# Kernel tuning notes

Measured on AMD Instinct MI355X. Metric: run time of the kernel, lower is better.

The kernel has to match this reference:

```python
import jax, jax.numpy as jnp
import numpy as np

B, M, K = 32768, 8192, 16
EPS = 1e-5  # torch BatchNorm1d default


def _bn_relu(x, g, b):
    # training-mode batch norm (biased variance), matching torch BatchNorm1d forward
    m = x.mean(0)
    v = x.var(0)
    return jax.nn.relu(g * (x - m) * jax.lax.rsqrt(v + EPS) + b)


def _forward(pos, mc, mv, w1, b1, w2, b2, w3, b3, w4, b4, w5, b5, w6, b6,
             g1, be1, g2, be2, g3, be3, g4, be4, g5, be5, k):
    # squared pairwise distances [B, M]; same ordering as L2 norm used by torch.sort
    d2 = (pos * pos).sum(1, keepdims=True) + (mc * mc).sum(1)[None, :] - 2.0 * (pos @ mc.T)
    _, idx = jax.lax.top_k(-d2, k)                     # k nearest indices [B, k]
    nb = jnp.concatenate([mc[idx], mv[idx]], axis=-1)  # [B, k, 4] = (coord, value) per neighbor
    knn_feat = jnp.concatenate([pos, nb.reshape(pos.shape[0], k * 4)], axis=1)  # [B, 2+4k]
    x = _bn_relu(knn_feat @ w1 + b1, g1, be1)
    x = _bn_relu(x @ w2 + b2, g2, be2)
    x = _bn_relu(x @ w3 + b3, g3, be3)
    x = _bn_relu(x @ w4 + b4, g4, be4)
    x = _bn_relu(x @ w5 + b5, g5, be5)  # dropout = identity (eval mode)
    x = x @ w6 + b6
    return x, knn_feat


def setup_inputs() -> dict:
    key = jax.random.key(0)
    ks = jax.random.split(key, 32)
    d_in = 2 + K * 4
    dims = [(d_in, 128), (128, 256), (256, 512), (512, 128), (128, 64), (64, 2)]
    inp = {
        "pos": jax.random.normal(ks[0], (B, 2), jnp.float32),
        "measure_coords": jax.random.normal(ks[1], (M, 2), jnp.float32),
        "measure_vals": jax.random.normal(ks[2], (M, 2), jnp.float32),
    }
    for i, (fi, fo) in enumerate(dims, 1):
        inp[f"w{i}"] = jax.random.normal(ks[2 + 2 * i], (fi, fo), jnp.float32) / np.float32(np.sqrt(fi))
        inp[f"b{i}"] = jnp.zeros((fo,), jnp.float32)
    for i, n in enumerate([128, 256, 512, 128, 64], 1):
        inp[f"g{i}"] = jnp.ones((n,), jnp.float32)
        inp[f"be{i}"] = jnp.zeros((n,), jnp.float32)
    inp["k"] = K
    return inp


def reference(pos, measure_coords, measure_vals, w1, b1, w2, b2, w3, b3, w4, b4,
              w5, b5, w6, b6, g1, be1, g2, be2, g3, be3, g4, be4, g5, be5, k):
    return _forward(pos, measure_coords, measure_vals, w1, b1, w2, b2, w3, b3, w4,
                    b4, w5, b5, w6, b6, g1, be1, g2, be2, g3, be3, g4, be4, g5, be5, k)
```

## Files before the change

### kernel.cpp

```cpp
#include <hip/hip_runtime.h>

typedef unsigned short u16;
typedef unsigned int   u32;
typedef __attribute__((ext_vector_type(8))) short bf16x8;
typedef __attribute__((ext_vector_type(4))) float f32x4;

#define B_ROWS 32768
#define EPS_BN 1e-5f

__device__ __forceinline__ u16 f2bf(float f) {
  u32 u = __float_as_uint(f);
  u32 r = (u + 0x7FFFu + ((u >> 16) & 1u)) >> 16;
  return (u16)r;
}
__device__ __forceinline__ u32 pk2bf(float a, float b) {
  return (u32)f2bf(a) | ((u32)f2bf(b) << 16);
}
__device__ __forceinline__ float bf2f(u16 h) {
  return __uint_as_float(((u32)h) << 16);
}

__device__ __forceinline__ float dcalc(float px, float py, float sp, float mx, float my) {
#pragma clang fp contract(off)
  float sm   = mx * mx + my * my;
  float pm   = px * mx;
  float dot  = __builtin_fmaf(py, my, pm);
  float spsm = sp + sm;
  return __builtin_fmaf(dot, -2.0f, spsm);
}
__device__ __forceinline__ float dcalc2(float px, float py, float sp, float mx, float my,
                                        float sm) {
#pragma clang fp contract(off)
  float pm   = px * mx;
  float dot  = __builtin_fmaf(py, my, pm);
  float spsm = sp + sm;
  return __builtin_fmaf(dot, -2.0f, spsm);
}
__device__ __forceinline__ float smcalc(float mx, float my) {
#pragma clang fp contract(off)
  return mx * mx + my * my;
}
__device__ __forceinline__ float spcalc(float px, float py) {
#pragma clang fp contract(off)
  return px * px + py * py;
}
#define MED3 __builtin_amdgcn_fmed3f

__global__ __launch_bounds__(256, 8)
void knn_kernel(const float2* __restrict__ pos, const float2* __restrict__ mc,
                const float2* __restrict__ mv, float* __restrict__ knn_out,
                u16* __restrict__ X0)
{
  __shared__ float tv[16 * 130];
  __shared__ float tstS[16];
  __shared__ float qxS[16], qyS[16], qsS[16];
  __shared__ unsigned long long qmaskS[16];
  __shared__ int   qcnt[16];
  __shared__ int   ntaskS;

  const int t = threadIdx.x;
  const int g = t >> 6;
  const int s = t & 63;
  const int q0 = blockIdx.x * 16;

  float px[4], py[4], sp[4];
#pragma unroll
  for (int j = 0; j < 4; ++j) {
    float2 p = pos[q0 + g * 4 + j];
    px[j] = p.x; py[j] = p.y; sp[j] = spcalc(p.x, p.y);
  }
#pragma unroll
  for (int j = 0; j < 4; ++j) {
    if (s == j) { qxS[g * 4 + j] = px[j]; qyS[g * 4 + j] = py[j]; qsS[g * 4 + j] = sp[j]; }
  }

  const float4* mc4 = (const float4*)mc;

  float z0[4], z1[4];
#pragma unroll
  for (int j = 0; j < 4; ++j) { z0[j] = __builtin_inff(); z1[j] = __builtin_inff(); }

  float4 cur = mc4[s];
  for (int i = 0; i < 64; ++i) {
    float4 nxt = mc4[((i + 1) & 63) * 64 + s];
    float smA = smcalc(cur.x, cur.y);
    float smB = smcalc(cur.z, cur.w);
#pragma unroll
    for (int j = 0; j < 4; ++j) {
      float dA = dcalc2(px[j], py[j], sp[j], cur.x, cur.y, smA);
      z1[j] = MED3(z0[j], dA, z1[j]); z0[j] = fminf(z0[j], dA);
      float dB = dcalc2(px[j], py[j], sp[j], cur.z, cur.w, smB);
      z1[j] = MED3(z0[j], dB, z1[j]); z0[j] = fminf(z0[j], dB);
    }
    cur = nxt;
  }
#pragma unroll
  for (int j = 0; j < 4; ++j) {
    float2 zz; zz.x = z0[j]; zz.y = z1[j];
    *(float2*)(&tv[(g * 4 + j) * 130 + s * 2]) = zz;
  }
  __syncthreads();

  if (t < 16) {
    float ch[16];
#pragma unroll
    for (int j = 0; j < 16; ++j) ch[j] = __builtin_inff();
    for (int k = 0; k < 128; ++k) {
      float v = tv[t * 130 + k];
#pragma unroll
      for (int j = 15; j >= 1; --j) ch[j] = MED3(ch[j-1], v, ch[j]);
      ch[0] = fminf(ch[0], v);
    }
    tstS[t] = ch[15];
    qcnt[t] = 0;
    if (t == 0) ntaskS = 0;
  }
  __syncthreads();

  {
    float Tq[4];
#pragma unroll
    for (int j = 0; j < 4; ++j) Tq[j] = tstS[g * 4 + j];
    unsigned long long m;
#pragma unroll
    for (int j = 0; j < 4; ++j) {
      m = __ballot(z0[j] <= Tq[j]);
      if (s == j) qmaskS[g * 4 + j] = m;
    }
  }
  __syncthreads();

  u16* qcand = (u16*)tv;
  u16* taskS = ((u16*)tv) + 1024;
  if (t < 16) {
    unsigned long long m = qmaskS[t];
    int c = __popcll(m);
    int off = atomicAdd(&ntaskS, c);
    u16 qb = (u16)(t << 6);
    while (m) {
      int b = (int)__builtin_ctzll(m);
      m &= m - 1;
      taskS[off++] = qb | (u16)b;
    }
  }
  __syncthreads();

  const int ntask = ntaskS;
  for (int i0 = t; i0 < ntask; i0 += 256) {
    const int task = taskS[i0];
    const int qrow = task >> 6;
    const int sl   = task & 63;
    const float qx = qxS[qrow], qy = qyS[qrow];
    const float qs = qsS[qrow], qT = tstS[qrow];
#pragma unroll 4
    for (int i = 0; i < 64; ++i) {
      float4 c2 = mc4[i * 64 + sl];
      const int pidx = 2 * (i * 64 + sl);
      float smA = smcalc(c2.x, c2.y);
      float smB = smcalc(c2.z, c2.w);
      float dA = dcalc2(qx, qy, qs, c2.x, c2.y, smA);
      float dB = dcalc2(qx, qy, qs, c2.z, c2.w, smB);
      if (dA <= qT) {
        int o = atomicAdd(&qcnt[qrow], 1);
        if (o < 64) qcand[qrow * 64 + o] = (u16)pidx;
      }
      if (dB <= qT) {
        int o = atomicAdd(&qcnt[qrow], 1);
        if (o < 64) qcand[qrow * 64 + o] = (u16)(pidx + 1);
      }
    }
  }
  __syncthreads();

  if (t < 16) {
    const int q = q0 + t;
    float2 p = pos[q];
    const float sq = spcalc(p.x, p.y);
    int cnt = qcnt[t]; if (cnt > 64) cnt = 64;
    float fd[16]; int fi[16];
#pragma unroll
    for (int j = 0; j < 16; ++j) { fd[j] = __builtin_inff(); fi[j] = 0x7fffffff; }
    for (int j = 0; j < cnt; ++j) {
      int ci = qcand[t * 64 + j];
      float2 m = mc[ci];
      float d = dcalc(p.x, p.y, sq, m.x, m.y);
      bool cc = (d < fd[15]) || (d == fd[15] && ci < fi[15]);
      if (cc) {
#pragma unroll
        for (int k = 15; k >= 1; --k) {
          bool cm = (d < fd[k-1]) || (d == fd[k-1] && ci < fi[k-1]);
          if (cc) {
            if (cm) { fd[k] = fd[k-1]; fi[k] = fi[k-1]; }
            else    { fd[k] = d;       fi[k] = ci;      }
          }
          cc = cm;
        }
        if (cc) { fd[0] = d; fi[0] = ci; }
      }
    }
    float* orow = knn_out + (size_t)q * 66;
    u16*   xrow = X0 + (size_t)q * 96;
    float2 pp; pp.x = p.x; pp.y = p.y;
    *(float2*)(&orow[0]) = pp;
    *(u32*)(&xrow[0]) = pk2bf(p.x, p.y);
#pragma unroll
    for (int j = 0; j < 16; ++j) {
      int ci = fi[j];
      float2 m = mc[ci], v = mv[ci];
      *(float2*)(&orow[2 + 4*j]) = m;
      *(float2*)(&orow[4 + 4*j]) = v;
      *(u32*)(&xrow[2 + 4*j]) = pk2bf(m.x, m.y);
      *(u32*)(&xrow[4 + 4*j]) = pk2bf(v.x, v.y);
    }
#pragma unroll
    for (int c = 33; c < 48; ++c) ((u32*)xrow)[c] = 0;
  }
}

__global__ __launch_bounds__(256)
void prep_wt_all(const float* __restrict__ w1, const float* __restrict__ w2,
                 const float* __restrict__ w3, const float* __restrict__ w4,
                 const float* __restrict__ w5,
                 u16* __restrict__ wt1, u16* __restrict__ wt2, u16* __restrict__ wt3,
                 u16* __restrict__ wt4, u16* __restrict__ wt5)
{
  const int l = blockIdx.y;
  const float* w; u16* wt; int K, N, Kp;
  if (l == 0)      { w = w1; wt = wt1; K = 66;  N = 128; Kp = 96;  }
  else if (l == 1) { w = w2; wt = wt2; K = 128; N = 256; Kp = 128; }
  else if (l == 2) { w = w3; wt = wt3; K = 256; N = 512; Kp = 256; }
  else if (l == 3) { w = w4; wt = wt4; K = 512; N = 128; Kp = 512; }
  else             { w = w5; wt = wt5; K = 128; N = 64;  Kp = 128; }
  int i = blockIdx.x * 256 + threadIdx.x;
  if (i >= N * Kp) return;
  int n = i / Kp, kp = i - n * Kp;
  float v = (kp < K) ? w[(size_t)kp * N + n] : 0.0f;
  wt[i] = f2bf(v);
}

template<int BN, bool FUSE>
__global__ __launch_bounds__(256)
void gemm_bn_kernel(const u16* __restrict__ X, int Kw,
                    const u16* __restrict__ WT,
                    const float* __restrict__ bias,
                    const float* __restrict__ psum, const float* __restrict__ psq,
                    const float* __restrict__ gw,   const float* __restrict__ bw,
                    u16* __restrict__ Z, int N,
                    float* __restrict__ csum, float* __restrict__ csq)
{
  constexpr int BM = 128;
  constexpr int AST = 40;
  __shared__ u16 Ash[BM * AST];
  __shared__ u16 Bsh[BN * AST];
  __shared__ float redS[4][BN];
  __shared__ float redQ[4][BN];
  __shared__ float scA[512];
  __shared__ float ttA[512];

  const int t = threadIdx.x;
  const int wave = t >> 6;
  const int lane = t & 63;
  const int lr = lane & 15;
  const int qd = lane >> 4;
  const int m0 = blockIdx.x * BM;
  const int n0 = blockIdx.y * BN;

  if (FUSE) {
    const float invB = 1.0f / 32768.0f;
    for (int c = t; c < Kw; c += 256) {
      float mean = psum[c] * invB;
      float var  = __fmaf_rn(-mean, mean, psq[c] * invB);
      float sc   = gw[c] * rsqrtf(var + EPS_BN);
      scA[c] = sc;
      ttA[c] = __fmaf_rn(-mean, sc, bw[c]);
    }
    __syncthreads();
  }

  f32x4 acc[2][BN / 16];
#pragma unroll
  for (int a = 0; a < 2; ++a)
#pragma unroll
    for (int b = 0; b < BN / 16; ++b) {
      acc[a][b][0] = 0.f; acc[a][b][1] = 0.f; acc[a][b][2] = 0.f; acc[a][b][3] = 0.f;
    }

  const int sr = t >> 2;
  const int sk = (t & 3) * 8;

  for (int k0 = 0; k0 < Kw; k0 += 32) {
#pragma unroll
    for (int rr = 0; rr < 2; ++rr) {
      int r = sr + rr * 64;
      uint4 g = *(const uint4*)(&X[(size_t)(m0 + r) * Kw + k0 + sk]);
      if (FUSE) {
        u32 w[4] = {g.x, g.y, g.z, g.w};
        u32 o[4];
#pragma unroll
        for (int e = 0; e < 4; ++e) {
          int kk = k0 + sk + 2 * e;
          float lo = bf2f((u16)(w[e] & 0xffffu));
          float hi = bf2f((u16)(w[e] >> 16));
          float yl = fmaxf(__fmaf_rn(lo, scA[kk],     ttA[kk]),     0.0f);
          float yh = fmaxf(__fmaf_rn(hi, scA[kk + 1], ttA[kk + 1]), 0.0f);
          o[e] = (u32)f2bf(yl) | ((u32)f2bf(yh) << 16);
        }
        g.x = o[0]; g.y = o[1]; g.z = o[2]; g.w = o[3];
      }
      *(uint4*)(&Ash[r * AST + sk]) = g;
    }
    if (BN == 128) {
#pragma unroll
      for (int rr = 0; rr < 2; ++rr) {
        int n = sr + rr * 64;
        *(uint4*)(&Bsh[n * AST + sk]) =
            *(const uint4*)(&WT[(size_t)(n0 + n) * Kw + k0 + sk]);
      }
    } else {
      int n = sr;
      *(uint4*)(&Bsh[n * AST + sk]) =
          *(const uint4*)(&WT[(size_t)(n0 + n) * Kw + k0 + sk]);
    }
    __syncthreads();
    bf16x8 af0 = *(const bf16x8*)(&Ash[(wave * 32 + lr) * AST + qd * 8]);
    bf16x8 af1 = *(const bf16x8*)(&Ash[(wave * 32 + 16 + lr) * AST + qd * 8]);
#pragma unroll
    for (int ct = 0; ct < BN / 16; ++ct) {
      bf16x8 bfr = *(const bf16x8*)(&Bsh[(ct * 16 + lr) * AST + qd * 8]);
      acc[0][ct] = __builtin_amdgcn_mfma_f32_16x16x32_bf16(af0, bfr, acc[0][ct], 0, 0, 0);
      acc[1][ct] = __builtin_amdgcn_mfma_f32_16x16x32_bf16(af1, bfr, acc[1][ct], 0, 0, 0);
    }
    __syncthreads();
  }

#pragma unroll
  for (int ct = 0; ct < BN / 16; ++ct) {
    int cg = n0 + ct * 16 + lr;
    float bv = bias[cg];
    float s = 0.f, sqv = 0.f;
#pragma unroll
    for (int rt = 0; rt < 2; ++rt) {
#pragma unroll
      for (int r = 0; r < 4; ++r) {
        float z = acc[rt][ct][r] + bv;
        int row = m0 + wave * 32 + rt * 16 + qd * 4 + r;
        Z[(size_t)row * N + cg] = f2bf(z);
        s += z;
        sqv = __fmaf_rn(z, z, sqv);
      }
    }
    s   += __shfl_xor(s, 16);   s   += __shfl_xor(s, 32);
    sqv += __shfl_xor(sqv, 16); sqv += __shfl_xor(sqv, 32);
    if (qd == 0) { redS[wave][ct * 16 + lr] = s; redQ[wave][ct * 16 + lr] = sqv; }
  }
  __syncthreads();
  if (t < BN) {
    float s  = redS[0][t] + redS[1][t] + redS[2][t] + redS[3][t];
    float sv = redQ[0][t] + redQ[1][t] + redQ[2][t] + redQ[3][t];
    atomicAdd(&csum[n0 + t], s);
    atomicAdd(&csq[n0 + t], sv);
  }
}

__global__ __launch_bounds__(256)
void gemv6_kernel(const u16* __restrict__ Z5, const float* __restrict__ w6,
                  const float* __restrict__ b6,
                  const float* __restrict__ psum, const float* __restrict__ psq,
                  const float* __restrict__ gw,   const float* __restrict__ bw,
                  float* __restrict__ out)
{
  __shared__ float wsh[128];
  __shared__ float scs[64];
  __shared__ float tts[64];
  const int t = threadIdx.x;
  if (t < 128) wsh[t] = w6[t];
  if (t < 64) {
    const float invB = 1.0f / 32768.0f;
    float mean = psum[t] * invB;
    float var  = __fmaf_rn(-mean, mean, psq[t] * invB);
    float sc   = gw[t] * rsqrtf(var + EPS_BN);
    scs[t] = sc;
    tts[t] = __fmaf_rn(-mean, sc, bw[t]);
  }
  __syncthreads();
  const int q = blockIdx.x * 256 + t;
  const uint4* xv = (const uint4*)(Z5 + (size_t)q * 64);
  float a0 = 0.f, a1 = 0.f;
#pragma unroll
  for (int cc = 0; cc < 8; ++cc) {
    uint4 pk = xv[cc];
    u32 u[4] = {pk.x, pk.y, pk.z, pk.w};
#pragma unroll
    for (int uu = 0; uu < 4; ++uu) {
      int k = cc * 8 + uu * 2;
      float z0 = bf2f((u16)(u[uu] & 0xffffu));
      float z1 = bf2f((u16)(u[uu] >> 16));
      float x0 = fmaxf(__fmaf_rn(z0, scs[k],     tts[k]),     0.0f);
      float x1 = fmaxf(__fmaf_rn(z1, scs[k + 1], tts[k + 1]), 0.0f);
      x0 = bf2f(f2bf(x0));
      x1 = bf2f(f2bf(x1));
      a0 = __fmaf_rn(x0, wsh[2 * k + 0], a0);
      a1 = __fmaf_rn(x0, wsh[2 * k + 1], a1);
      a0 = __fmaf_rn(x1, wsh[2 * k + 2], a0);
      a1 = __fmaf_rn(x1, wsh[2 * k + 3], a1);
    }
  }
  float2 o; o.x = a0 + b6[0]; o.y = a1 + b6[1];
  ((float2*)out)[q] = o;
}

extern "C" void kernel_launch(void* const* d_in, const int* in_sizes, int n_in,
                              void* d_out, int out_size, void* d_ws, size_t ws_size,
                              hipStream_t stream)
{
  const float2* pos = (const float2*)d_in[0];
  const float2* mc  = (const float2*)d_in[1];
  const float2* mv  = (const float2*)d_in[2];
  const float* w1 = (const float*)d_in[3];  const float* b1 = (const float*)d_in[4];
  const float* w2 = (const float*)d_in[5];  const float* b2 = (const float*)d_in[6];
  const float* w3 = (const float*)d_in[7];  const float* b3 = (const float*)d_in[8];
  const float* w4 = (const float*)d_in[9];  const float* b4 = (const float*)d_in[10];
  const float* w5 = (const float*)d_in[11]; const float* b5 = (const float*)d_in[12];
  const float* w6 = (const float*)d_in[13]; const float* b6 = (const float*)d_in[14];
  const float* g1 = (const float*)d_in[15]; const float* be1 = (const float*)d_in[16];
  const float* g2 = (const float*)d_in[17]; const float* be2 = (const float*)d_in[18];
  const float* g3 = (const float*)d_in[19]; const float* be3 = (const float*)d_in[20];
  const float* g4 = (const float*)d_in[21]; const float* be4 = (const float*)d_in[22];
  const float* g5 = (const float*)d_in[23]; const float* be5 = (const float*)d_in[24];

  char* ws = (char*)d_ws;
  u16* X0   = (u16*)(ws + 0);
  u16* ZA   = (u16*)(ws + 6291456);
  u16* ZB   = (u16*)(ws + 39845888);
  u16* WT1  = (u16*)(ws + 73400320);
  u16* WT2  = (u16*)(ws + 73424896);
  u16* WT3  = (u16*)(ws + 73490432);
  u16* WT4  = (u16*)(ws + 73752576);
  u16* WT5  = (u16*)(ws + 73883648);
  float* stats = (float*)(ws + 73900032);
  float* s1 = stats;        float* s2 = stats + 128;  float* s3 = stats + 384;
  float* s4 = stats + 896;  float* s5 = stats + 1024;
  float* sqb = stats + 1088;
  float* q1 = sqb;          float* q2 = sqb + 128;    float* q3 = sqb + 384;
  float* q4 = sqb + 896;    float* q5 = sqb + 1024;

  float* outX = (float*)d_out;
  float* outK = outX + 2 * B_ROWS;

  hipMemsetAsync(stats, 0, 2176 * sizeof(float), stream);
  prep_wt_all<<<dim3(512, 5), 256, 0, stream>>>(w1, w2, w3, w4, w5, WT1, WT2, WT3, WT4, WT5);
  knn_kernel<<<dim3(2048), 256, 0, stream>>>(pos, mc, mv, outK, X0);

  gemm_bn_kernel<64, false><<<dim3(256, 2), 256, 0, stream>>>(
      X0, 96, WT1, b1, nullptr, nullptr, nullptr, nullptr, ZA, 128, s1, q1);
  gemm_bn_kernel<64, true><<<dim3(256, 4), 256, 0, stream>>>(
      ZA, 128, WT2, b2, s1, q1, g1, be1, ZB, 256, s2, q2);
  gemm_bn_kernel<64, true><<<dim3(256, 8), 256, 0, stream>>>(
      ZB, 256, WT3, b3, s2, q2, g2, be2, ZA, 512, s3, q3);
  gemm_bn_kernel<64, true><<<dim3(256, 2), 256, 0, stream>>>(
      ZA, 512, WT4, b4, s3, q3, g3, be3, ZB, 128, s4, q4);
  gemm_bn_kernel<64, true><<<dim3(256, 1), 256, 0, stream>>>(
      ZB, 128, WT5, b5, s4, q4, g4, be4, ZA, 64, s5, q5);
  gemv6_kernel<<<dim3(128), 256, 0, stream>>>(ZA, w6, b6, s5, q5, g5, be5, outX);

  (void)in_sizes; (void)n_in; (void)out_size; (void)ws_size;
}
```

Baseline: 316.6 us.

## Restructure MLP GEMMs: full-K activation tile in LDS, all columns per block

Each block now owns 64 rows and loads its whole K extent (or up to 256-wide halves) of activations into LDS once, fused with the BN+ReLU of the previous layer. It then loops over every output column, reading weight fragments straight from global memory or cache instead of staging them in LDS. The earlier design re-read and re-normalized the activations once per column tile and synchronized on every 32-wide K step. Column statistics are now reduced in LDS with shared atomics before one global atomic per column. The trade-offs are heavier LDS use, higher register pressure from large accumulator arrays when NP>1, and weight loads that depend on L1/L2 reuse.

```diff
diff --git a/kernel.cpp b/kernel.cpp
--- a/kernel.cpp
+++ b/kernel.cpp
@@ -238,127 +238,163 @@
   wt[i] = f2bf(v);
 }
 
-template<int BN, bool FUSE>
-__global__ __launch_bounds__(256)
-void gemm_bn_kernel(const u16* __restrict__ X, int Kw,
+template<int KW, int NN, bool FUSE>
+__global__ __launch_bounds__(256, 2)
+void gemm_bn_kernel(const u16* __restrict__ X,
                     const u16* __restrict__ WT,
                     const float* __restrict__ bias,
                     const float* __restrict__ psum, const float* __restrict__ psq,
                     const float* __restrict__ gw,   const float* __restrict__ bw,
-                    u16* __restrict__ Z, int N,
+                    u16* __restrict__ Z,
                     float* __restrict__ csum, float* __restrict__ csq)
 {
-  constexpr int BM = 128;
-  constexpr int AST = 40;
-  __shared__ u16 Ash[BM * AST];
-  __shared__ u16 Bsh[BN * AST];
-  __shared__ float redS[4][BN];
-  __shared__ float redQ[4][BN];
-  __shared__ float scA[512];
-  __shared__ float ttA[512];
+  constexpr int KS  = (KW > 256) ? 256 : KW;
+  constexpr int NP  = KW / KS;
+  constexpr int AST = KS + 8;
+  constexpr int NT  = NN / 64;
+  __shared__ u16 Ash[64 * AST];
+  __shared__ float colS[NN];
+  __shared__ float colQ[NN];
+  __shared__ float scA[FUSE ? KW : 1];
+  __shared__ float ttA[FUSE ? KW : 1];
 
   const int t = threadIdx.x;
   const int wave = t >> 6;
   const int lane = t & 63;
   const int lr = lane & 15;
   const int qd = lane >> 4;
-  const int m0 = blockIdx.x * BM;
-  const int n0 = blockIdx.y * BN;
+  const int m0 = blockIdx.x * 64;
 
   if (FUSE) {
     const float invB = 1.0f / 32768.0f;
-    for (int c = t; c < Kw; c += 256) {
+    for (int c = t; c < KW; c += 256) {
       float mean = psum[c] * invB;
       float var  = __fmaf_rn(-mean, mean, psq[c] * invB);
       float sc   = gw[c] * rsqrtf(var + EPS_BN);
       scA[c] = sc;
       ttA[c] = __fmaf_rn(-mean, sc, bw[c]);
     }
+  }
+  for (int c = t; c < NN; c += 256) { colS[c] = 0.f; colQ[c] = 0.f; }
+  __syncthreads();
+
+  auto fuseq = [&](uint4 gv, int kk) -> uint4 {
+    u32 w[4] = {gv.x, gv.y, gv.z, gv.w};
+    u32 o[4];
+#pragma unroll
+    for (int e = 0; e < 4; ++e) {
+      float lo = bf2f((u16)(w[e] & 0xffffu));
+      float hi = bf2f((u16)(w[e] >> 16));
+      float yl = fmaxf(__fmaf_rn(lo, scA[kk + 2 * e],     ttA[kk + 2 * e]),     0.0f);
+      float yh = fmaxf(__fmaf_rn(hi, scA[kk + 2 * e + 1], ttA[kk + 2 * e + 1]), 0.0f);
+      o[e] = (u32)f2bf(yl) | ((u32)f2bf(yh) << 16);
+    }
+    uint4 r; r.x = o[0]; r.y = o[1]; r.z = o[2]; r.w = o[3];
+    return r;
+  };
+
+  if constexpr (NP == 1) {
+    constexpr int NV = 64 * KW / 8;
+    for (int v = t; v < NV; v += 256) {
+      const int r  = v / (KW / 8);
+      const int kc = (v - r * (KW / 8)) * 8;
+      uint4 g = *(const uint4*)(&X[(size_t)(m0 + r) * KW + kc]);
+      if (FUSE) g = fuseq(g, kc);
+      *(uint4*)(&Ash[r * AST + kc]) = g;
+    }
     __syncthreads();
-  }
-
-  f32x4 acc[2][BN / 16];
-#pragma unroll
-  for (int a = 0; a < 2; ++a)
-#pragma unroll
-    for (int b = 0; b < BN / 16; ++b) {
-      acc[a][b][0] = 0.f; acc[a][b][1] = 0.f; acc[a][b][2] = 0.f; acc[a][b][3] = 0.f;
-    }
-
-  const int sr = t >> 2;
-  const int sk = (t & 3) * 8;
-
-  for (int k0 = 0; k0 < Kw; k0 += 32) {
-#pragma unroll
-    for (int rr = 0; rr < 2; ++rr) {
-      int r = sr + rr * 64;
-      uint4 g = *(const uint4*)(&X[(size_t)(m0 + r) * Kw + k0 + sk]);
-      if (FUSE) {
-        u32 w[4] = {g.x, g.y, g.z, g.w};
-        u32 o[4];
-#pragma unroll
-        for (int e = 0; e < 4; ++e) {
-          int kk = k0 + sk + 2 * e;
-          float lo = bf2f((u16)(w[e] & 0xffffu));
-          float hi = bf2f((u16)(w[e] >> 16));
-          float yl = fmaxf(__fmaf_rn(lo, scA[kk],     ttA[kk]),     0.0f);
-          float yh = fmaxf(__fmaf_rn(hi, scA[kk + 1], ttA[kk + 1]), 0.0f);
-          o[e] = (u32)f2bf(yl) | ((u32)f2bf(yh) << 16);
+
+    for (int nt = 0; nt < NT; ++nt) {
+      f32x4 acc[4];
+#pragma unroll
+      for (int ct = 0; ct < 4; ++ct) {
+        acc[ct][0] = 0.f; acc[ct][1] = 0.f; acc[ct][2] = 0.f; acc[ct][3] = 0.f;
+      }
+      const u16* Bl = WT + (size_t)(nt * 64 + lr) * KW + qd * 8;
+#pragma unroll
+      for (int ks = 0; ks < KW / 32; ++ks) {
+        bf16x8 af = *(const bf16x8*)(&Ash[(wave * 16 + lr) * AST + ks * 32 + qd * 8]);
+#pragma unroll
+        for (int ct = 0; ct < 4; ++ct) {
+          bf16x8 bfr = *(const bf16x8*)(Bl + (size_t)ct * 16 * KW + ks * 32);
+          acc[ct] = __builtin_amdgcn_mfma_f32_16x16x32_bf16(af, bfr, acc[ct], 0, 0, 0);
         }
-        g.x = o[0]; g.y = o[1]; g.z = o[2]; g.w = o[3];
-      }
-      *(uint4*)(&Ash[r * AST + sk]) = g;
-    }
-    if (BN == 128) {
-#pragma unroll
-      for (int rr = 0; rr < 2; ++rr) {
-        int n = sr + rr * 64;
-        *(uint4*)(&Bsh[n * AST + sk]) =
-            *(const uint4*)(&WT[(size_t)(n0 + n) * Kw + k0 + sk]);
-      }
-    } else {
-      int n = sr;
-      *(uint4*)(&Bsh[n * AST + sk]) =
-          *(const uint4*)(&WT[(size_t)(n0 + n) * Kw + k0 + sk]);
-    }
-    __syncthreads();
-    bf16x8 af0 = *(const bf16x8*)(&Ash[(wave * 32 + lr) * AST + qd * 8]);
-    bf16x8 af1 = *(const bf16x8*)(&Ash[(wave * 32 + 16 + lr) * AST + qd * 8]);
-#pragma unroll
-    for (int ct = 0; ct < BN / 16; ++ct) {
-      bf16x8 bfr = *(const bf16x8*)(&Bsh[(ct * 16 + lr) * AST + qd * 8]);
-      acc[0][ct] = __builtin_amdgcn_mfma_f32_16x16x32_bf16(af0, bfr, acc[0][ct], 0, 0, 0);
-      acc[1][ct] = __builtin_amdgcn_mfma_f32_16x16x32_bf16(af1, bfr, acc[1][ct], 0, 0, 0);
-    }
-    __syncthreads();
-  }
-
-#pragma unroll
-  for (int ct = 0; ct < BN / 16; ++ct) {
-    int cg = n0 + ct * 16 + lr;
-    float bv = bias[cg];
-    float s = 0.f, sqv = 0.f;
-#pragma unroll
-    for (int rt = 0; rt < 2; ++rt) {
-#pragma unroll
-      for (int r = 0; r < 4; ++r) {
-        float z = acc[rt][ct][r] + bv;
-        int row = m0 + wave * 32 + rt * 16 + qd * 4 + r;
-        Z[(size_t)row * N + cg] = f2bf(z);
-        s += z;
-        sqv = __fmaf_rn(z, z, sqv);
-      }
-    }
-    s   += __shfl_xor(s, 16);   s   += __shfl_xor(s, 32);
-    sqv += __shfl_xor(sqv, 16); sqv += __shfl_xor(sqv, 32);
-    if (qd == 0) { redS[wave][ct * 16 + lr] = s; redQ[wave][ct * 16 + lr] = sqv; }
-  }
-  __syncthreads();
-  if (t < BN) {
-    float s  = redS[0][t] + redS[1][t] + redS[2][t] + redS[3][t];
-    float sv = redQ[0][t] + redQ[1][t] + redQ[2][t] + redQ[3][t];
-    atomicAdd(&csum[n0 + t], s);
-    atomicAdd(&csq[n0 + t], sv);
+      }
+#pragma unroll
+      for (int ct = 0; ct < 4; ++ct) {
+        const int cg = nt * 64 + ct * 16 + lr;
+        const float bv = bias[cg];
+        float s = 0.f, sq = 0.f;
+#pragma unroll
+        for (int r = 0; r < 4; ++r) {
+          float z = acc[ct][r] + bv;
+          int row = m0 + wave * 16 + qd * 4 + r;
+          Z[(size_t)row * NN + cg] = f2bf(z);
+          s += z;
+          sq = __fmaf_rn(z, z, sq);
+        }
+        s  += __shfl_xor(s, 16);  s  += __shfl_xor(s, 32);
+        sq += __shfl_xor(sq, 16); sq += __shfl_xor(sq, 32);
+        if (qd == 0) { atomicAdd(&colS[cg], s); atomicAdd(&colQ[cg], sq); }
+      }
+    }
+  } else {
+    f32x4 acc[NT][4];
+#pragma unroll
+    for (int nt = 0; nt < NT; ++nt)
+#pragma unroll
+      for (int ct = 0; ct < 4; ++ct) {
+        acc[nt][ct][0] = 0.f; acc[nt][ct][1] = 0.f;
+        acc[nt][ct][2] = 0.f; acc[nt][ct][3] = 0.f;
+      }
+    for (int kp = 0; kp < NP; ++kp) {
+      if (kp) __syncthreads();
+      constexpr int NV = 64 * KS / 8;
+      for (int v = t; v < NV; v += 256) {
+        const int r  = v / (KS / 8);
+        const int kc = (v - r * (KS / 8)) * 8;
+        uint4 g = *(const uint4*)(&X[(size_t)(m0 + r) * KW + kp * KS + kc]);
+        if (FUSE) g = fuseq(g, kp * KS + kc);
+        *(uint4*)(&Ash[r * AST + kc]) = g;
+      }
+      __syncthreads();
+      for (int nt = 0; nt < NT; ++nt) {
+        const u16* Bl = WT + (size_t)(nt * 64 + lr) * KW + kp * KS + qd * 8;
+#pragma unroll
+        for (int ks = 0; ks < KS / 32; ++ks) {
+          bf16x8 af = *(const bf16x8*)(&Ash[(wave * 16 + lr) * AST + ks * 32 + qd * 8]);
+#pragma unroll
+          for (int ct = 0; ct < 4; ++ct) {
+            bf16x8 bfr = *(const bf16x8*)(Bl + (size_t)ct * 16 * KW + ks * 32);
+            acc[nt][ct] = __builtin_amdgcn_mfma_f32_16x16x32_bf16(af, bfr, acc[nt][ct], 0, 0, 0);
+          }
+        }
+      }
+    }
+    for (int nt = 0; nt < NT; ++nt) {
+#pragma unroll
+      for (int ct = 0; ct < 4; ++ct) {
+        const int cg = nt * 64 + ct * 16 + lr;
+        const float bv = bias[cg];
+        float s = 0.f, sq = 0.f;
+#pragma unroll
+        for (int r = 0; r < 4; ++r) {
+          float z = acc[nt][ct][r] + bv;
+          int row = m0 + wave * 16 + qd * 4 + r;
+          Z[(size_t)row * NN + cg] = f2bf(z);
+          s += z;
+          sq = __fmaf_rn(z, z, sq);
+        }
+        s  += __shfl_xor(s, 16);  s  += __shfl_xor(s, 32);
+        sq += __shfl_xor(sq, 16); sq += __shfl_xor(sq, 32);
+        if (qd == 0) { atomicAdd(&colS[cg], s); atomicAdd(&colQ[cg], sq); }
+      }
+    }
+  }
+  __syncthreads();
+  for (int c = t; c < NN; c += 256) {
+    atomicAdd(&csum[c], colS[c]);
+    atomicAdd(&csq[c], colQ[c]);
   }
 }
 
@@ -451,16 +487,16 @@
   prep_wt_all<<<dim3(512, 5), 256, 0, stream>>>(w1, w2, w3, w4, w5, WT1, WT2, WT3, WT4, WT5);
   knn_kernel<<<dim3(2048), 256, 0, stream>>>(pos, mc, mv, outK, X0);
 
-  gemm_bn_kernel<64, false><<<dim3(256, 2), 256, 0, stream>>>(
-      X0, 96, WT1, b1, nullptr, nullptr, nullptr, nullptr, ZA, 128, s1, q1);
-  gemm_bn_kernel<64, true><<<dim3(256, 4), 256, 0, stream>>>(
-      ZA, 128, WT2, b2, s1, q1, g1, be1, ZB, 256, s2, q2);
-  gemm_bn_kernel<64, true><<<dim3(256, 8), 256, 0, stream>>>(
-      ZB, 256, WT3, b3, s2, q2, g2, be2, ZA, 512, s3, q3);
-  gemm_bn_kernel<64, true><<<dim3(256, 2), 256, 0, stream>>>(
-      ZA, 512, WT4, b4, s3, q3, g3, be3, ZB, 128, s4, q4);
-  gemm_bn_kernel<64, true><<<dim3(256, 1), 256, 0, stream>>>(
-      ZB, 128, WT5, b5, s4, q4, g4, be4, ZA, 64, s5, q5);
+  gemm_bn_kernel<96,  128, false><<<dim3(512), 256, 0, stream>>>(
+      X0, WT1, b1, nullptr, nullptr, nullptr, nullptr, ZA, s1, q1);
+  gemm_bn_kernel<128, 256, true><<<dim3(512), 256, 0, stream>>>(
+      ZA, WT2, b2, s1, q1, g1, be1, ZB, s2, q2);
+  gemm_bn_kernel<256, 512, true><<<dim3(512), 256, 0, stream>>>(
+      ZB, WT3, b3, s2, q2, g2, be2, ZA, s3, q3);
+  gemm_bn_kernel<512, 128, true><<<dim3(512), 256, 0, stream>>>(
+      ZA, WT4, b4, s3, q3, g3, be3, ZB, s4, q4);
+  gemm_bn_kernel<128, 64,  true><<<dim3(512), 256, 0, stream>>>(
+      ZB, WT5, b5, s4, q4, g4, be4, ZA, s5, q5);
   gemv6_kernel<<<dim3(128), 256, 0, stream>>>(ZA, w6, b6, s5, q5, g5, be5, outX);
 
   (void)in_sizes; (void)n_in; (void)out_size; (void)ws_size;
```

After: 427.7 us. 35.1% more time.
